# Optimization experiments

Hardware: AMD Instinct MI355X
Metric: run time of the kernel (lower is better)

The kernel has to match this reference:

```python
import jax, jax.numpy as jnp
import numpy as np

B, N, IN_F = 8, 1024, 128
H, FH = 4, 32
NEG_SLOPE = 0.2


def setup_inputs() -> dict:
    key = jax.random.key(0)
    k_x, k_adj, k_w, k_a = jax.random.split(key, 4)
    x = jax.random.normal(k_x, (B, N, IN_F), dtype=jnp.float32)
    adj_raw = jax.random.uniform(k_adj, (B, N, N), dtype=jnp.float32)
    adj = jnp.where(adj_raw < 0.5, 0.0, adj_raw)
    # nn.Linear(in, out*H, bias=False): weight shape [H*FH, IN_F]
    W_weight = jax.random.normal(k_w, (H * FH, IN_F), dtype=jnp.float32) * 0.1
    # attn param: [H, 2*FH + 1] (use_edge_feat=True)
    attn = jax.random.normal(k_a, (H, 2 * FH + 1), dtype=jnp.float32) * 0.1
    return {"x": x, "adj": adj, "W_weight": W_weight, "attn": attn}


def reference(x, adj, W_weight, attn):
    # h = W(x): [B, N, H, FH]
    h = jnp.einsum("bni,oi->bno", x, W_weight).reshape(B, N, H, FH)
    # decompose a^T [h_i || h_j || A_ij] = a_src.h_i + a_dst.h_j + a_e*A_ij
    a_src = attn[:, :FH]            # [H, FH]
    a_dst = attn[:, FH:2 * FH]      # [H, FH]
    a_e = attn[:, 2 * FH]           # [H]
    src = jnp.einsum("bnhf,hf->bnh", h, a_src)   # score for node as i
    dst = jnp.einsum("bnhf,hf->bnh", h, a_dst)   # score for node as j
    # e[b,i,j,h]
    e = src[:, :, None, :] + dst[:, None, :, :] + adj[..., None] * a_e
    e = jnp.where(e >= 0, e, NEG_SLOPE * e)      # LeakyReLU
    no_edge = (adj == 0.0)[..., None]            # [B, N, N, 1]
    e = jnp.where(no_edge, -jnp.inf, e)
    alpha = jax.nn.softmax(e, axis=2)            # softmax over j
    alpha = jnp.nan_to_num(alpha, nan=0.0)
    # dropout: eval mode -> identity
    # out[b,i,h,f] = sum_j alpha[b,i,j,h] * h[b,j,h,f]
    out = jnp.einsum("bijh,bjhf->bihf", alpha, h).reshape(B, N, H * FH)
    return out, alpha
```

## Files before the change

### kernel.cpp

```cpp
#include <hip/hip_runtime.h>

#define NEG 0.2f
constexpr int B_ = 8, N_ = 1024;

__global__ __launch_bounds__(256) void gat_h_kernel(
    const float* __restrict__ x, const float* __restrict__ Ww,
    const float* __restrict__ attn,
    float* __restrict__ hfeat, float* __restrict__ srcv, float* __restrict__ dstv)
{
    __shared__ float Wl[128 * 128];
    const int tid = threadIdx.x;
    const int row0 = blockIdx.x * 16;

    #pragma unroll
    for (int k = 0; k < 16; ++k) {
        int f = tid + k * 256;
        int o = f >> 5, ib = f & 31;
        float4 w = *(const float4*)(Ww + o * 128 + ib * 4);
        *(float4*)&Wl[o * 128 + ((ib ^ ((o >> 2) & 7)) << 2)] = w;
    }
    __syncthreads();

    const int colg = tid & 31;
    const int rg   = tid >> 5;
    const int swz  = colg & 7;
    float acc[2][4] = {};
    const float* xr = x + (size_t)(row0 + rg * 2) * 128;

    #pragma unroll 8
    for (int is = 0; is < 32; ++is) {
        float4 x0 = *(const float4*)(xr + is * 4);
        float4 x1 = *(const float4*)(xr + 128 + is * 4);
        #pragma unroll
        for (int cc = 0; cc < 4; ++cc) {
            float4 wv = *(const float4*)&Wl[(colg * 4 + cc) * 128 + ((is ^ swz) << 2)];
            acc[0][cc] = fmaf(x0.x, wv.x, acc[0][cc]);
            acc[0][cc] = fmaf(x0.y, wv.y, acc[0][cc]);
            acc[0][cc] = fmaf(x0.z, wv.z, acc[0][cc]);
            acc[0][cc] = fmaf(x0.w, wv.w, acc[0][cc]);
            acc[1][cc] = fmaf(x1.x, wv.x, acc[1][cc]);
            acc[1][cc] = fmaf(x1.y, wv.y, acc[1][cc]);
            acc[1][cc] = fmaf(x1.z, wv.z, acc[1][cc]);
            acc[1][cc] = fmaf(x1.w, wv.w, acc[1][cc]);
        }
    }
    #pragma unroll
    for (int r = 0; r < 2; ++r) {
        float4 hv = make_float4(acc[r][0], acc[r][1], acc[r][2], acc[r][3]);
        *(float4*)(hfeat + (size_t)(row0 + rg * 2 + r) * 128 + colg * 4) = hv;
    }
    const int hh = colg >> 3;
    float ps[2] = {0.f, 0.f}, pd[2] = {0.f, 0.f};
    #pragma unroll
    for (int cc = 0; cc < 4; ++cc) {
        int fi = (colg & 7) * 4 + cc;
        float as = attn[hh * 65 + fi];
        float ad = attn[hh * 65 + 32 + fi];
        ps[0] = fmaf(acc[0][cc], as, ps[0]); ps[1] = fmaf(acc[1][cc], as, ps[1]);
        pd[0] = fmaf(acc[0][cc], ad, pd[0]); pd[1] = fmaf(acc[1][cc], ad, pd[1]);
    }
    #pragma unroll
    for (int m = 1; m <= 4; m <<= 1) {
        ps[0] += __shfl_xor(ps[0], m); ps[1] += __shfl_xor(ps[1], m);
        pd[0] += __shfl_xor(pd[0], m); pd[1] += __shfl_xor(pd[1], m);
    }
    if ((tid & 7) == 0) {
        #pragma unroll
        for (int r = 0; r < 2; ++r) {
            srcv[(size_t)(row0 + rg * 2 + r) * 4 + hh] = ps[r];
            dstv[(size_t)(row0 + rg * 2 + r) * 4 + hh] = pd[r];
        }
    }
}

__global__ __launch_bounds__(512, 4) void gat_attn_kernel(
    const float* __restrict__ adj, const float* __restrict__ attn,
    const float* __restrict__ hfeat, const float* __restrict__ srcv,
    const float* __restrict__ dstv,
    float* __restrict__ out, float* __restrict__ alpha)
{
    __shared__ float src_l[64];
    __shared__ float rs_l[64];
    __shared__ float al_l[4 * 64 * 21];
    __shared__ float h_t[64 * 128];

    const int tid  = threadIdx.x;
    const int lane = tid & 63;
    const int w    = tid >> 6;
    const int b    = blockIdx.x & 7;
    const int i0   = (blockIdx.x >> 3) * 16;

    float aE[4];
    #pragma unroll
    for (int h = 0; h < 4; ++h) aE[h] = attn[h * 65 + 64];

    if (tid < 64) src_l[tid] = srcv[(size_t)(b * N_ + i0) * 4 + tid];
    __syncthreads();

    const float* dstb = dstv + (size_t)b * N_ * 4;
    #pragma unroll
    for (int rr = 0; rr < 2; ++rr) {
        int row = w * 2 + rr;
        const float* arow = adj + ((size_t)(b * N_ + i0 + row)) * N_;
        float sd[4];
        #pragma unroll
        for (int h = 0; h < 4; ++h) sd[h] = src_l[row * 4 + h];
        float s[4] = {0.f, 0.f, 0.f, 0.f};
        #pragma unroll
        for (int k = 0; k < 4; ++k) {
            float4 av4 = *(const float4*)(arow + lane * 4 + k * 256);
            const float* avp = (const float*)&av4;
            #pragma unroll
            for (int q = 0; q < 4; ++q) {
                float av = avp[q];
                if (av != 0.f) {
                    int j = lane * 4 + k * 256 + q;
                    float4 dv = *(const float4*)(dstb + j * 4);
                    const float* dvp = (const float*)&dv;
                    #pragma unroll
                    for (int h = 0; h < 4; ++h) {
                        float e = fmaf(av, aE[h], sd[h] + dvp[h]);
                        e = e >= 0.f ? e : NEG * e;
                        s[h] += __expf(e);
                    }
                }
            }
        }
        #pragma unroll
        for (int m = 1; m <= 32; m <<= 1) {
            #pragma unroll
            for (int h = 0; h < 4; ++h) s[h] += __shfl_xor(s[h], m);
        }
        if (lane == 0) {
            #pragma unroll
            for (int h = 0; h < 4; ++h)
                rs_l[row * 4 + h] = s[h] > 0.f ? 1.f / s[h] : 0.f;
        }
    }

    const int rhalf  = w & 1;
    const int hh     = w >> 1;
    const int hf8low = (lane >> 4) & 3;
    const int jc     = lane & 15;
    float4 acc[8][2];
    #pragma unroll
    for (int r = 0; r < 8; ++r) {
        acc[r][0] = make_float4(0.f, 0.f, 0.f, 0.f);
        acc[r][1] = make_float4(0.f, 0.f, 0.f, 0.f);
    }

    for (int jt = 0; jt < 16; ++jt) {
        const int j0 = jt * 64;
        __syncthreads();
        #pragma unroll
        for (int k = 0; k < 4; ++k) {
            int f = tid + k * 512;
            int jj = f >> 5, cb = f & 31;
            float4 hv = *(const float4*)(hfeat + (size_t)(b * N_ + j0 + jj) * 128 + cb * 4);
            *(float4*)&h_t[jj * 128 + ((cb ^ (jj & 7)) << 2)] = hv;
        }
        #pragma unroll
        for (int t = 0; t < 2; ++t) {
            int r = w + t * 8;
            float av = adj[((size_t)(b * N_ + i0 + r)) * N_ + j0 + lane];
            float4 al = make_float4(0.f, 0.f, 0.f, 0.f);
            if (av != 0.f) {
                float4 dv = *(const float4*)(dstb + (j0 + lane) * 4);
                const float* dvp = (const float*)&dv;
                float* alp = (float*)&al;
                #pragma unroll
                for (int h = 0; h < 4; ++h) {
                    float e = fmaf(av, aE[h], src_l[r * 4 + h] + dvp[h]);
                    e = e >= 0.f ? e : NEG * e;
                    alp[h] = __expf(e) * rs_l[r * 4 + h];
                }
            }
            const float* alp = (const float*)&al;
            #pragma unroll
            for (int h = 0; h < 4; ++h)
                al_l[h * 1344 + lane * 21 + r] = alp[h];
            *(float4*)(alpha + (((size_t)(b * N_ + i0 + r)) * N_ + j0 + lane) * 4) = al;
        }
        __syncthreads();
        #pragma unroll
        for (int s = 0; s < 4; ++s) {
            int jj = s * 16 + jc;
            const float* ab = &al_l[hh * 1344 + jj * 21 + rhalf * 8];
            float av8[8];
            #pragma unroll
            for (int ri = 0; ri < 8; ++ri) av8[ri] = ab[ri];
            int cb0 = hh * 8 + hf8low * 2;
            float4 v0 = *(const float4*)&h_t[jj * 128 + ((cb0 ^ (jj & 7)) << 2)];
            float4 v1 = *(const float4*)&h_t[jj * 128 + (((cb0 + 1) ^ (jj & 7)) << 2)];
#define PVROW(RR, AV)                                                    \
            acc[RR][0].x = fmaf(AV, v0.x, acc[RR][0].x);                 \
            acc[RR][0].y = fmaf(AV, v0.y, acc[RR][0].y);                 \
            acc[RR][0].z = fmaf(AV, v0.z, acc[RR][0].z);                 \
            acc[RR][0].w = fmaf(AV, v0.w, acc[RR][0].w);                 \
            acc[RR][1].x = fmaf(AV, v1.x, acc[RR][1].x);                 \
            acc[RR][1].y = fmaf(AV, v1.y, acc[RR][1].y);                 \
            acc[RR][1].z = fmaf(AV, v1.z, acc[RR][1].z);                 \
            acc[RR][1].w = fmaf(AV, v1.w, acc[RR][1].w);
            PVROW(0, av8[0]) PVROW(1, av8[1]) PVROW(2, av8[2]) PVROW(3, av8[3])
            PVROW(4, av8[4]) PVROW(5, av8[5]) PVROW(6, av8[6]) PVROW(7, av8[7])
#undef PVROW
        }
    }

    #pragma unroll
    for (int m = 1; m <= 8; m <<= 1) {
        #pragma unroll
        for (int r = 0; r < 8; ++r) {
            #pragma unroll
            for (int c = 0; c < 2; ++c) {
                acc[r][c].x += __shfl_xor(acc[r][c].x, m);
                acc[r][c].y += __shfl_xor(acc[r][c].y, m);
                acc[r][c].z += __shfl_xor(acc[r][c].z, m);
                acc[r][c].w += __shfl_xor(acc[r][c].w, m);
            }
        }
    }
    #pragma unroll
    for (int r = 0; r < 8; ++r) {
        #pragma unroll
        for (int c = 0; c < 2; ++c) {
            if ((jc >> 1) == r && (jc & 1) == c) {
                int orow = i0 + rhalf * 8 + r;
                int ocol = hh * 32 + hf8low * 8 + c * 4;
                *(float4*)(out + (size_t)(b * N_ + orow) * 128 + ocol) = acc[r][c];
            }
        }
    }
}

extern "C" void kernel_launch(void* const* d_in, const int* in_sizes, int n_in,
                              void* d_out, int out_size, void* d_ws, size_t ws_size,
                              hipStream_t stream) {
    const float* x    = (const float*)d_in[0];
    const float* adj  = (const float*)d_in[1];
    const float* Ww   = (const float*)d_in[2];
    const float* attn = (const float*)d_in[3];

    float* out   = (float*)d_out;
    float* alpha = out + (size_t)B_ * N_ * 128;

    float* hfeat = (float*)d_ws;
    float* srcv  = hfeat + (size_t)B_ * N_ * 128;
    float* dstv  = srcv + (size_t)B_ * N_ * 4;

    gat_h_kernel<<<512, 256, 0, stream>>>(x, Ww, attn, hfeat, srcv, dstv);
    gat_attn_kernel<<<512, 512, 0, stream>>>(adj, attn, hfeat, srcv, dstv, out, alpha);
}
```

Measured before the change: 279.9 us.

## Halve rows per attention block, drop LDS h tile, prefetch adj with nontemporal ops

The attention kernel now processes 8 query rows per block instead of 16 and launches twice as many blocks with a higher occupancy hint. The shared h_t staging tile is removed, and h features are read straight from global memory, relying on cache. The next adj chunk is prefetched across the barrier, and the adj loads and alpha stores use nontemporal hints to avoid polluting cache. The aim is more parallelism and overlap of the memory-bound alpha write. The cost is that hfeat reuse per block drops, so global/L2 traffic for h doubles.

Result: slower. 303.3 us (+8.4%).

```diff
diff --git a/kernel.cpp b/kernel.cpp
--- a/kernel.cpp
+++ b/kernel.cpp
@@ -1,4 +1,6 @@
 #include <hip/hip_runtime.h>
+
+typedef float f4 __attribute__((ext_vector_type(4)));
 
 #define NEG 0.2f
 constexpr int B_ = 8, N_ = 1024;
@@ -73,53 +75,48 @@
     }
 }
 
-__global__ __launch_bounds__(512, 4) void gat_attn_kernel(
+__global__ __launch_bounds__(512, 8) void gat_attn_kernel(
     const float* __restrict__ adj, const float* __restrict__ attn,
     const float* __restrict__ hfeat, const float* __restrict__ srcv,
     const float* __restrict__ dstv,
     float* __restrict__ out, float* __restrict__ alpha)
 {
-    __shared__ float src_l[64];
-    __shared__ float rs_l[64];
-    __shared__ float al_l[4 * 64 * 21];
-    __shared__ float h_t[64 * 128];
+    __shared__ float src_l[32];
+    __shared__ float rs_l[32];
+    __shared__ float al_l[4 * 64 * 12];
 
     const int tid  = threadIdx.x;
     const int lane = tid & 63;
     const int w    = tid >> 6;
     const int b    = blockIdx.x & 7;
-    const int i0   = (blockIdx.x >> 3) * 16;
+    const int i0   = (blockIdx.x >> 3) * 8;
 
     float aE[4];
     #pragma unroll
     for (int h = 0; h < 4; ++h) aE[h] = attn[h * 65 + 64];
 
-    if (tid < 64) src_l[tid] = srcv[(size_t)(b * N_ + i0) * 4 + tid];
+    if (tid < 32) src_l[tid] = srcv[(size_t)(b * N_ + i0) * 4 + tid];
     __syncthreads();
 
     const float* dstb = dstv + (size_t)b * N_ * 4;
-    #pragma unroll
-    for (int rr = 0; rr < 2; ++rr) {
-        int row = w * 2 + rr;
-        const float* arow = adj + ((size_t)(b * N_ + i0 + row)) * N_;
+    const float* arow = adj + ((size_t)(b * N_ + i0 + w)) * N_;
+    {
         float sd[4];
         #pragma unroll
-        for (int h = 0; h < 4; ++h) sd[h] = src_l[row * 4 + h];
+        for (int h = 0; h < 4; ++h) sd[h] = src_l[w * 4 + h];
         float s[4] = {0.f, 0.f, 0.f, 0.f};
         #pragma unroll
         for (int k = 0; k < 4; ++k) {
-            float4 av4 = *(const float4*)(arow + lane * 4 + k * 256);
-            const float* avp = (const float*)&av4;
+            f4 av4 = __builtin_nontemporal_load((const f4*)(arow + lane * 4 + k * 256));
             #pragma unroll
             for (int q = 0; q < 4; ++q) {
-                float av = avp[q];
+                float av = av4[q];
                 if (av != 0.f) {
                     int j = lane * 4 + k * 256 + q;
-                    float4 dv = *(const float4*)(dstb + j * 4);
-                    const float* dvp = (const float*)&dv;
+                    f4 dv = *(const f4*)(dstb + j * 4);
                     #pragma unroll
                     for (int h = 0; h < 4; ++h) {
-                        float e = fmaf(av, aE[h], sd[h] + dvp[h]);
+                        float e = fmaf(av, aE[h], sd[h] + dv[h]);
                         e = e >= 0.f ? e : NEG * e;
                         s[h] += __expf(e);
                     }
@@ -134,102 +131,73 @@
         if (lane == 0) {
             #pragma unroll
             for (int h = 0; h < 4; ++h)
-                rs_l[row * 4 + h] = s[h] > 0.f ? 1.f / s[h] : 0.f;
-        }
-    }
-
-    const int rhalf  = w & 1;
-    const int hh     = w >> 1;
-    const int hf8low = (lane >> 4) & 3;
-    const int jc     = lane & 15;
-    float4 acc[8][2];
-    #pragma unroll
-    for (int r = 0; r < 8; ++r) {
-        acc[r][0] = make_float4(0.f, 0.f, 0.f, 0.f);
-        acc[r][1] = make_float4(0.f, 0.f, 0.f, 0.f);
-    }
+                rs_l[w * 4 + h] = s[h] > 0.f ? 1.f / s[h] : 0.f;
+        }
+    }
+
+    const int hh    = w >> 1;
+    const int chalf = w & 1;
+    const int jc    = lane & 15;
+    const int colq  = lane >> 4;
+    const int hcol  = hh * 32 + chalf * 16 + colq * 4;
+    f4 acc[8];
+    #pragma unroll
+    for (int r = 0; r < 8; ++r) acc[r] = (f4)0.f;
+
+    float* alrow = alpha + ((size_t)(b * N_ + i0 + w)) * N_ * 4;
+    float av_cur = __builtin_nontemporal_load(arow + lane);
+    float av_next = 0.f;
 
     for (int jt = 0; jt < 16; ++jt) {
         const int j0 = jt * 64;
+        f4 al = (f4)0.f;
+        if (av_cur != 0.f) {
+            f4 dv  = *(const f4*)(dstb + (j0 + lane) * 4);
+            f4 sdv = *(const f4*)&src_l[w * 4];
+            f4 rsv = *(const f4*)&rs_l[w * 4];
+            #pragma unroll
+            for (int h = 0; h < 4; ++h) {
+                float e = fmaf(av_cur, aE[h], sdv[h] + dv[h]);
+                e = e >= 0.f ? e : NEG * e;
+                al[h] = __expf(e) * rsv[h];
+            }
+        }
+        #pragma unroll
+        for (int h = 0; h < 4; ++h)
+            al_l[h * 768 + lane * 12 + w] = al[h];
+        __builtin_nontemporal_store(al, (f4*)(alrow + (j0 + lane) * 4));
         __syncthreads();
-        #pragma unroll
-        for (int k = 0; k < 4; ++k) {
-            int f = tid + k * 512;
-            int jj = f >> 5, cb = f & 31;
-            float4 hv = *(const float4*)(hfeat + (size_t)(b * N_ + j0 + jj) * 128 + cb * 4);
-            *(float4*)&h_t[jj * 128 + ((cb ^ (jj & 7)) << 2)] = hv;
-        }
-        #pragma unroll
-        for (int t = 0; t < 2; ++t) {
-            int r = w + t * 8;
-            float av = adj[((size_t)(b * N_ + i0 + r)) * N_ + j0 + lane];
-            float4 al = make_float4(0.f, 0.f, 0.f, 0.f);
-            if (av != 0.f) {
-                float4 dv = *(const float4*)(dstb + (j0 + lane) * 4);
-                const float* dvp = (const float*)&dv;
-                float* alp = (float*)&al;
-                #pragma unroll
-                for (int h = 0; h < 4; ++h) {
-                    float e = fmaf(av, aE[h], src_l[r * 4 + h] + dvp[h]);
-                    e = e >= 0.f ? e : NEG * e;
-                    alp[h] = __expf(e) * rs_l[r * 4 + h];
-                }
-            }
-            const float* alp = (const float*)&al;
-            #pragma unroll
-            for (int h = 0; h < 4; ++h)
-                al_l[h * 1344 + lane * 21 + r] = alp[h];
-            *(float4*)(alpha + (((size_t)(b * N_ + i0 + r)) * N_ + j0 + lane) * 4) = al;
-        }
-        __syncthreads();
+        if (jt < 15) av_next = __builtin_nontemporal_load(arow + j0 + 64 + lane);
         #pragma unroll
         for (int s = 0; s < 4; ++s) {
             int jj = s * 16 + jc;
-            const float* ab = &al_l[hh * 1344 + jj * 21 + rhalf * 8];
-            float av8[8];
-            #pragma unroll
-            for (int ri = 0; ri < 8; ++ri) av8[ri] = ab[ri];
-            int cb0 = hh * 8 + hf8low * 2;
-            float4 v0 = *(const float4*)&h_t[jj * 128 + ((cb0 ^ (jj & 7)) << 2)];
-            float4 v1 = *(const float4*)&h_t[jj * 128 + (((cb0 + 1) ^ (jj & 7)) << 2)];
-#define PVROW(RR, AV)                                                    \
-            acc[RR][0].x = fmaf(AV, v0.x, acc[RR][0].x);                 \
-            acc[RR][0].y = fmaf(AV, v0.y, acc[RR][0].y);                 \
-            acc[RR][0].z = fmaf(AV, v0.z, acc[RR][0].z);                 \
-            acc[RR][0].w = fmaf(AV, v0.w, acc[RR][0].w);                 \
-            acc[RR][1].x = fmaf(AV, v1.x, acc[RR][1].x);                 \
-            acc[RR][1].y = fmaf(AV, v1.y, acc[RR][1].y);                 \
-            acc[RR][1].z = fmaf(AV, v1.z, acc[RR][1].z);                 \
-            acc[RR][1].w = fmaf(AV, v1.w, acc[RR][1].w);
-            PVROW(0, av8[0]) PVROW(1, av8[1]) PVROW(2, av8[2]) PVROW(3, av8[3])
-            PVROW(4, av8[4]) PVROW(5, av8[5]) PVROW(6, av8[6]) PVROW(7, av8[7])
-#undef PVROW
-        }
+            const float* ab = &al_l[hh * 768 + jj * 12];
+            f4 avA = *(const f4*)ab;
+            f4 avB = *(const f4*)(ab + 4);
+            f4 hv = *(const f4*)(hfeat + (size_t)(b * N_ + j0 + jj) * 128 + hcol);
+            acc[0] += avA.x * hv; acc[1] += avA.y * hv;
+            acc[2] += avA.z * hv; acc[3] += avA.w * hv;
+            acc[4] += avB.x * hv; acc[5] += avB.y * hv;
+            acc[6] += avB.z * hv; acc[7] += avB.w * hv;
+        }
+        __syncthreads();
+        av_cur = av_next;
     }
 
     #pragma unroll
     for (int m = 1; m <= 8; m <<= 1) {
         #pragma unroll
         for (int r = 0; r < 8; ++r) {
-            #pragma unroll
-            for (int c = 0; c < 2; ++c) {
-                acc[r][c].x += __shfl_xor(acc[r][c].x, m);
-                acc[r][c].y += __shfl_xor(acc[r][c].y, m);
-                acc[r][c].z += __shfl_xor(acc[r][c].z, m);
-                acc[r][c].w += __shfl_xor(acc[r][c].w, m);
-            }
+            acc[r].x += __shfl_xor(acc[r].x, m);
+            acc[r].y += __shfl_xor(acc[r].y, m);
+            acc[r].z += __shfl_xor(acc[r].z, m);
+            acc[r].w += __shfl_xor(acc[r].w, m);
         }
     }
     #pragma unroll
     for (int r = 0; r < 8; ++r) {
-        #pragma unroll
-        for (int c = 0; c < 2; ++c) {
-            if ((jc >> 1) == r && (jc & 1) == c) {
-                int orow = i0 + rhalf * 8 + r;
-                int ocol = hh * 32 + hf8low * 8 + c * 4;
-                *(float4*)(out + (size_t)(b * N_ + orow) * 128 + ocol) = acc[r][c];
-            }
-        }
+        if (jc == r)
+            *(f4*)(out + (size_t)(b * N_ + i0 + r) * 128 + hcol) = acc[r];
     }
 }
 
@@ -249,5 +217,5 @@
     float* dstv  = srcv + (size_t)B_ * N_ * 4;
 
     gat_h_kernel<<<512, 256, 0, stream>>>(x, Ww, attn, hfeat, srcv, dstv);
-    gat_attn_kernel<<<512, 512, 0, stream>>>(adj, attn, hfeat, srcv, dstv, out, alpha);
+    gat_attn_kernel<<<1024, 512, 0, stream>>>(adj, attn, hfeat, srcv, dstv, out, alpha);
 }
```
